# Kernel tuning notes

Measured on AMD Instinct MI355X. Metric: run time of the kernel, lower is better.

Reference implementation:

```python
import jax, jax.numpy as jnp
import numpy as np

DIM = 2048
N_HEADS = 16
N_KV_HEADS = 8
HEAD_DIM = DIM // N_HEADS  # 128
N_REP = N_HEADS // N_KV_HEADS
THETA = 10000.0


def _rope_cos_sin(seq_len, head_dim):
    # freqs_cis = polar(1, outer(t, 1/theta^(2i/d))), i in [0, head_dim//2)
    inv = 1.0 / (THETA ** (jnp.arange(0, head_dim, 2, dtype=jnp.float32) / head_dim))
    t = jnp.arange(seq_len, dtype=jnp.float32)
    freqs = jnp.outer(t, inv)  # [S, hd/2]
    return jnp.cos(freqs), jnp.sin(freqs)


def _apply_rope(x, cos, sin):
    # x: [B, S, H, hd]; pairs (even, odd) treated as complex and multiplied by e^{i*freq}
    xr = x[..., 0::2]
    xi = x[..., 1::2]
    c = cos[None, :, None, :]
    s = sin[None, :, None, :]
    out_r = xr * c - xi * s
    out_i = xr * s + xi * c
    return jnp.stack([out_r, out_i], axis=-1).reshape(x.shape)


def setup_inputs() -> dict:
    key = jax.random.key(0)
    ks = jax.random.split(key, 5)
    B, S = 2, 2048
    sc = 0.02
    return {
        "x": jax.random.normal(ks[0], (B, S, DIM), dtype=jnp.float32),
        "wq": jax.random.normal(ks[1], (N_HEADS * HEAD_DIM, DIM), dtype=jnp.float32) * sc,
        "wk": jax.random.normal(ks[2], (N_KV_HEADS * HEAD_DIM, DIM), dtype=jnp.float32) * sc,
        "wv": jax.random.normal(ks[3], (N_KV_HEADS * HEAD_DIM, DIM), dtype=jnp.float32) * sc,
        "wo": jax.random.normal(ks[4], (DIM, N_HEADS * HEAD_DIM), dtype=jnp.float32) * sc,
        "start_pos": 0,
        "inference": 0,
    }


def reference(x, wq, wk, wv, wo, start_pos, inference):
    B, S, _ = x.shape
    xq = (x @ wq.T).reshape(B, S, N_HEADS, HEAD_DIM)
    xk = (x @ wk.T).reshape(B, S, N_KV_HEADS, HEAD_DIM)
    xv = (x @ wv.T).reshape(B, S, N_KV_HEADS, HEAD_DIM)

    cos, sin = _rope_cos_sin(S, HEAD_DIM)
    xq = _apply_rope(xq, cos, sin)
    xk = _apply_rope(xk, cos, sin)

    # repeat_kv (GQA): [B,S,Hkv,hd] -> [B,S,Hkv*n_rep,hd]
    xk = jnp.repeat(xk, N_REP, axis=2)
    xv = jnp.repeat(xv, N_REP, axis=2)

    q = xq.transpose(0, 2, 1, 3)  # [B,H,S,hd]
    k = xk.transpose(0, 2, 1, 3)
    v = xv.transpose(0, 2, 1, 3)

    scores = jnp.einsum("bhqd,bhkd->bhqk", q, k) / np.sqrt(HEAD_DIM).astype(np.float32)
    mask = jnp.triu(jnp.full((S, S), -jnp.inf, dtype=scores.dtype), k=1)
    scores = scores + mask
    probs = jax.nn.softmax(scores.astype(jnp.float32), axis=-1).astype(q.dtype)

    out = jnp.einsum("bhqk,bhkd->bhqd", probs, v)
    out = out.transpose(0, 2, 1, 3).reshape(B, S, N_HEADS * HEAD_DIM)
    return out @ wo.T
```

## Files before the change

kernel.cpp:

```cpp
#include <hip/hip_runtime.h>
#include <hip/hip_bf16.h>
#include <stdint.h>
#include <type_traits>

typedef __attribute__((ext_vector_type(4))) float   f32x4;
typedef __attribute__((ext_vector_type(8))) __bf16  bf16x8;
typedef __attribute__((ext_vector_type(4))) unsigned int u32x4;

#define B_   2
#define S_   2048
#define DIM_ 2048
#define NH_  16
#define NKV_ 8
#define HD_  128

__device__ inline unsigned short f2bf(float f) {
    unsigned u = __float_as_uint(f);
    unsigned r = (u + 0x7fffu + ((u >> 16) & 1u)) >> 16;
    return (unsigned short)r;
}
__device__ inline float bf2f(unsigned short s) {
    return __uint_as_float(((unsigned)s) << 16);
}

__global__ void k_convert(const float* __restrict__ x,  const float* __restrict__ wq,
                          const float* __restrict__ wk, const float* __restrict__ wv,
                          const float* __restrict__ wo,
                          unsigned short* __restrict__ xb,  unsigned short* __restrict__ wqkb,
                          unsigned short* __restrict__ wvb, unsigned short* __restrict__ wob)
{
    int i = blockIdx.x * blockDim.x + threadIdx.x;
    const int NX = 2097152, NWQ = 1048576, NWK = 524288, NWV = 524288, NWO = 1048576;
    const float* src; unsigned short* dst; int j = i;
    if (j < NX) { src = x; dst = xb; }
    else {
        j -= NX;
        if (j < NWQ) { src = wq; dst = wqkb; }
        else {
            j -= NWQ;
            if (j < NWK) { src = wk; dst = wqkb + (size_t)2048 * 2048; }
            else {
                j -= NWK;
                if (j < NWV) { src = wv; dst = wvb; }
                else { j -= NWV; if (j >= NWO) return; src = wo; dst = wob; }
            }
        }
    }
    float4 v = reinterpret_cast<const float4*>(src)[j];
    ushort4 o;
    o.x = f2bf(v.x); o.y = f2bf(v.y); o.z = f2bf(v.z); o.w = f2bf(v.w);
    reinterpret_cast<ushort4*>(dst)[j] = o;
}

__global__ void k_rope_table(float* __restrict__ tab)
{
    int t = blockIdx.x * blockDim.x + threadIdx.x;
    if (t >= S_ * 64) return;
    int i = t & 63;
    int s = t >> 6;
    float inv = expf(-((float)i / 64.0f) * 9.210340371976184f);
    float ang = (float)s * inv;
    tab[2 * t]     = cosf(ang);
    tab[2 * t + 1] = sinf(ang);
}


#define BAR  __builtin_amdgcn_s_barrier()
#define WLG  asm volatile("s_waitcnt lgkmcnt(0)" ::: "memory")
#define WVM4 asm volatile("s_waitcnt vmcnt(4)" ::: "memory")
#define WVM0 asm volatile("s_waitcnt vmcnt(0)" ::: "memory")

#define G_LDS(SRC, DST) __builtin_amdgcn_global_load_lds( \
    (const __attribute__((address_space(1))) void*)(SRC), \
    (__attribute__((address_space(3))) void*)(DST), 16, 0, 0)

#define STAGE(MATB, DBUF, HALF, KT) do { \
    const unsigned short* _s0 = ((MATB) ? pb0 : pa0) + (size_t)(HALF) * 128 * 2048 + (KT) * 64; \
    const unsigned short* _s1 = ((MATB) ? pb1 : pa1) + (size_t)(HALF) * 128 * 2048 + (KT) * 64; \
    G_LDS(_s0, lds + (MATB) * 32768 + (DBUF) * 16384 + (HALF) * 8192 + lo0); \
    G_LDS(_s1, lds + (MATB) * 32768 + (DBUF) * 16384 + (HALF) * 8192 + lo1); \
} while (0)

#define LDA(DBUF, MH) { \
    _Pragma("unroll") \
    for (int mf = 0; mf < 4; ++mf) { \
        _Pragma("unroll") \
        for (int kk = 0; kk < 2; ++kk) { \
            const int R = wm * 128 + (MH) * 64 + mf * 16 + lr; \
            afr[MH][mf][kk] = *reinterpret_cast<const bf16x8*>( \
                &lds[(DBUF) * 16384 + R * 64 + (((kk * 4 + g) ^ (lr & 7)) * 8)]); \
        } } }

#define LDB(DBUF, NH) { \
    _Pragma("unroll") \
    for (int nf = 0; nf < 2; ++nf) { \
        _Pragma("unroll") \
        for (int kk = 0; kk < 2; ++kk) { \
            const int R = wn * 64 + (NH) * 32 + nf * 16 + lr; \
            bfr[NH][nf][kk] = *reinterpret_cast<const bf16x8*>( \
                &lds[32768 + (DBUF) * 16384 + R * 64 + (((kk * 4 + g) ^ (lr & 7)) * 8)]); \
        } } }

#define MMA(MH, NH) { \
    __builtin_amdgcn_s_setprio(1); \
    _Pragma("unroll") \
    for (int mf = 0; mf < 4; ++mf) { \
        _Pragma("unroll") \
        for (int nf = 0; nf < 2; ++nf) { \
            _Pragma("unroll") \
            for (int kk = 0; kk < 2; ++kk) \
                acc[(MH) * 4 + mf][(NH) * 2 + nf] = __builtin_amdgcn_mfma_f32_16x16x32_bf16( \
                    afr[MH][mf][kk], bfr[NH][nf][kk], acc[(MH) * 4 + mf][(NH) * 2 + nf], 0, 0, 0); \
        } } \
    __builtin_amdgcn_s_setprio(0); }

template <int MODE>
__global__ __launch_bounds__(512, 2) void k_gemm256(
    const unsigned short* __restrict__ A0g, const unsigned short* __restrict__ B0g,
    const unsigned short* __restrict__ A1g, const unsigned short* __restrict__ B1g,
    unsigned short* __restrict__ Cq, unsigned short* __restrict__ Cv,
    float* __restrict__ Cf, const float* __restrict__ tab)
{
    __shared__ __attribute__((aligned(16))) unsigned short lds[65536];

    const int tid  = threadIdx.x;
    const int lane = tid & 63;
    const int wid  = tid >> 6;
    const int g    = lane >> 4;
    const int lr   = lane & 15;
    const int wm   = wid >> 2;
    const int wn   = wid & 3;

    const unsigned short *Ag, *Bg;
    int brow, bcol;
    bool isQK = true;
    if constexpr (MODE == 0) {
        int swz = (blockIdx.x & 7) * 32 + (blockIdx.x >> 3);
        if (swz < 192) { Ag = A0g; Bg = B0g; brow = (swz / 12) << 8; bcol = (swz % 12) << 8; }
        else { int ix = swz - 192; isQK = false; Ag = A1g; Bg = B1g; brow = (ix >> 4) << 8; bcol = (ix & 15) << 8; }
    } else {
        int swz = (blockIdx.x & 7) * 16 + (blockIdx.x >> 3);
        Ag = A0g; Bg = B0g; brow = (swz >> 3) << 8; bcol = (swz & 7) << 8;
    }

    const int E0 = wid * 512 + lane * 8;
    const int E1 = E0 + 4096;
    const int r0 = E0 >> 6, r1 = E1 >> 6;
    const int c0 = ((((E0 >> 3) & 7) ^ (r0 & 7)) * 8);
    const int c1 = ((((E1 >> 3) & 7) ^ (r1 & 7)) * 8);
    const unsigned short* pa0 = Ag + (size_t)(brow + r0) * 2048 + c0;
    const unsigned short* pa1 = Ag + (size_t)(brow + r1) * 2048 + c1;
    const unsigned short* pb0 = Bg + (size_t)(bcol + r0) * 2048 + c0;
    const unsigned short* pb1 = Bg + (size_t)(bcol + r1) * 2048 + c1;
    const int lo0 = wid * 512;
    const int lo1 = lo0 + 4096;

    f32x4 acc[8][4] = {};
    bf16x8 afr[2][4][2];
    bf16x8 bfr[2][2][2];

    STAGE(0, 0, 0, 0); STAGE(0, 0, 1, 0); STAGE(1, 0, 0, 0); STAGE(1, 0, 1, 0);
    STAGE(0, 1, 0, 1); STAGE(1, 1, 0, 1);
    WVM0; BAR;

    #pragma unroll 1
    for (int i = 0; i < 16; ++i) {
        const int kt1 = 2 * i + 1;
        int kt2 = 2 * i + 2;  if (kt2 >= 32) kt2 -= 32;
        int kt3 = 2 * i + 3;  if (kt3 >= 32) kt3 -= 32;
        LDA(0, 0); LDB(0, 0);
        STAGE(0, 1, 1, kt1);
        BAR; WLG; MMA(0, 0); BAR;
        LDA(0, 1);
        STAGE(1, 1, 1, kt1);
        BAR; WLG; MMA(1, 0); BAR;
        LDB(0, 1);
        STAGE(1, 0, 0, kt2);
        BAR; WLG; MMA(0, 1); BAR;
        STAGE(0, 0, 0, kt2);
        WVM4;
        BAR; WLG; MMA(1, 1); BAR;
        LDA(1, 0); LDB(1, 0);
        STAGE(0, 0, 1, kt2);
        BAR; WLG; MMA(0, 0); BAR;
        LDA(1, 1);
        STAGE(1, 0, 1, kt2);
        BAR; WLG; MMA(1, 0); BAR;
        LDB(1, 1);
        STAGE(1, 1, 0, kt3);
        BAR; WLG; MMA(0, 1); BAR;
        STAGE(0, 1, 0, kt3);
        WVM4;
        BAR; WLG; MMA(1, 1); BAR;
    }

    if constexpr (MODE == 1) {
        #pragma unroll
        for (int m = 0; m < 8; ++m)
            #pragma unroll
            for (int n = 0; n < 4; ++n)
                #pragma unroll
                for (int r = 0; r < 4; ++r) {
                    int row = brow + wm * 128 + (m >> 2) * 64 + (m & 3) * 16 + g * 4 + r;
                    int col = bcol + wn * 64 + (n >> 1) * 32 + (n & 1) * 16 + lr;
                    Cf[(size_t)row * 2048 + col] = acc[m][n][r];
                }
    } else if (isQK) {
        #pragma unroll
        for (int m = 0; m < 8; ++m) {
            #pragma unroll
            for (int n = 0; n < 4; ++n) {
                int col = bcol + wn * 64 + (n >> 1) * 32 + (n & 1) * 16 + lr;
                int ci  = (col & 127) >> 1;
                int row0 = brow + wm * 128 + (m >> 2) * 64 + (m & 3) * 16 + g * 4;
                #pragma unroll
                for (int r = 0; r < 4; ++r) {
                    int row = row0 + r;
                    int s   = row & (S_ - 1);
                    float2 cs = *reinterpret_cast<const float2*>(&tab[(s * 64 + ci) * 2]);
                    float v = acc[m][n][r];
                    float o = __shfl_xor(v, 1);
                    float res = (lane & 1) ? fmaf(o, cs.y, v * cs.x)
                                           : fmaf(v, cs.x, -(o * cs.y));
                    Cq[(size_t)row * 3072 + col] = f2bf(res);
                }
            }
        }
    } else {
        #pragma unroll
        for (int m = 0; m < 8; ++m)
            #pragma unroll
            for (int n = 0; n < 4; ++n)
                #pragma unroll
                for (int r = 0; r < 4; ++r) {
                    int row = brow + wm * 128 + (m >> 2) * 64 + (m & 3) * 16 + g * 4 + r;
                    int col = bcol + wn * 64 + (n >> 1) * 32 + (n & 1) * 16 + lr;
                    Cv[(size_t)row * 4096 + col] = f2bf(acc[m][n][r]);
                }
    }
}

__global__ __launch_bounds__(256, 2) void k_attn(
    const unsigned short* __restrict__ QK,
    const unsigned short* __restrict__ Vt,
    unsigned short* __restrict__ O)
{
    __shared__ __attribute__((aligned(16))) unsigned short Ks[64 * 128];
    __shared__ __attribute__((aligned(16))) unsigned short Vs[128 * 64];

    const int tid  = threadIdx.x;
    const int lane = tid & 63;
    const int wid  = tid >> 6;
    const int g    = lane >> 4;
    const int lr   = lane & 15;

    const int bid    = blockIdx.x;
    const int qt_raw = bid & 15;
    const int h      = (bid >> 4) & 15;
    const int b      = bid >> 8;
    const int qt     = b ? (15 - qt_raw) : qt_raw;
    const int hk     = h >> 1;
    const int q0w    = qt * 128 + wid * 32;

    bf16x8 qf[2][4];
    #pragma unroll
    for (int qb = 0; qb < 2; ++qb)
        #pragma unroll
        for (int c = 0; c < 4; ++c)
            qf[qb][c] = *reinterpret_cast<const bf16x8*>(
                QK + (size_t)(b * S_ + q0w + qb * 16 + lr) * 3072 + h * HD_ + c * 32 + g * 8);

    f32x4 o_acc[2][8] = {};
    float m_run[2] = {-INFINITY, -INFINITY};
    float l_run[2] = {0.f, 0.f};

    const float C2 = 1.4426950408889634f * 0.08838834764831845f;
    const int nt = 2 * qt + 2;
    const int srcb = (g & 1) * 32 + lr;
    const bool hig = g >> 1;

    for (int t = 0; t < nt; ++t) {
        const int kv0 = t * 64;
        __syncthreads();
        #pragma unroll
        for (int i4 = 0; i4 < 4; ++i4) {
            const int base = (i4 * 4 + wid) * 512;
            const int E = base + lane * 8;
            {
                int row = E >> 7, ch = (E >> 3) & 15;
                int col = ((ch ^ (row & 15)) * 8);
                __builtin_amdgcn_global_load_lds(
                    (const __attribute__((address_space(1))) void*)(
                        QK + (size_t)(b * S_ + kv0 + row) * 3072 + 2048 + hk * HD_ + col),
                    (__attribute__((address_space(3))) void*)(Ks + base), 16, 0, 0);
            }
            {
                int d = E >> 6, ch = (E >> 3) & 7;
                int kv = ((ch ^ (d & 7)) * 8);
                __builtin_amdgcn_global_load_lds(
                    (const __attribute__((address_space(1))) void*)(
                        Vt + (size_t)(hk * HD_ + d) * (B_ * S_) + b * S_ + kv0 + kv),
                    (__attribute__((address_space(3))) void*)(Vs + base), 16, 0, 0);
            }
        }
        __syncthreads();

        const bool active = kv0 < q0w + 32;
        if (active) {
            f32x4 sv[2][4] = {};
            #pragma unroll
            for (int c = 0; c < 4; ++c)
                #pragma unroll
                for (int kvb = 0; kvb < 4; ++kvb) {
                    bf16x8 kf = *reinterpret_cast<const bf16x8*>(
                        &Ks[(kvb * 16 + lr) * 128 + (((c * 4 + g) ^ lr) * 8)]);
                    #pragma unroll
                    for (int qb = 0; qb < 2; ++qb)
                        sv[qb][kvb] = __builtin_amdgcn_mfma_f32_16x16x32_bf16(
                            kf, qf[qb][c], sv[qb][kvb], 0, 0, 0);
                }

            if (kv0 + 63 > q0w) {
                #pragma unroll
                for (int qb = 0; qb < 2; ++qb) {
                    int qg = q0w + qb * 16 + lr;
                    #pragma unroll
                    for (int kvb = 0; kvb < 4; ++kvb) {
                        int kvg0 = kv0 + kvb * 16 + g * 4;
                        #pragma unroll
                        for (int r = 0; r < 4; ++r)
                            if (kvg0 + r > qg) sv[qb][kvb][r] = -INFINITY;
                    }
                }
            }

            float mt[2];
            #pragma unroll
            for (int qb = 0; qb < 2; ++qb) {
                float a  = fmaxf(fmaxf(sv[qb][0][0], sv[qb][0][1]), fmaxf(sv[qb][0][2], sv[qb][0][3]));
                float c2 = fmaxf(fmaxf(sv[qb][1][0], sv[qb][1][1]), fmaxf(sv[qb][1][2], sv[qb][1][3]));
                float c3 = fmaxf(fmaxf(sv[qb][2][0], sv[qb][2][1]), fmaxf(sv[qb][2][2], sv[qb][2][3]));
                float c4 = fmaxf(fmaxf(sv[qb][3][0], sv[qb][3][1]), fmaxf(sv[qb][3][2], sv[qb][3][3]));
                float m0 = fmaxf(fmaxf(a, c2), fmaxf(c3, c4));
                m0 = fmaxf(m0, __shfl_xor(m0, 16));
                m0 = fmaxf(m0, __shfl_xor(m0, 32));
                mt[qb] = m0;
            }

            bool need = (mt[0] > m_run[0] + 90.5f) | (mt[1] > m_run[1] + 90.5f);
            if (__any(need)) {
                #pragma unroll
                for (int qb = 0; qb < 2; ++qb) {
                    float mn = fmaxf(m_run[qb], mt[qb]);
                    float al = exp2f((m_run[qb] - mn) * C2);
                    m_run[qb] = mn;
                    l_run[qb] *= al;
                    #pragma unroll
                    for (int db = 0; db < 8; ++db)
                        #pragma unroll
                        for (int r = 0; r < 4; ++r)
                            o_acc[qb][db][r] *= al;
                }
            }

            unsigned pk[2][4][2];
            #pragma unroll
            for (int qb = 0; qb < 2; ++qb) {
                float mb2 = m_run[qb] * C2;
                float rs = 0.f;
                #pragma unroll
                for (int kvb = 0; kvb < 4; ++kvb) {
                    float p0 = exp2f(fmaf(sv[qb][kvb][0], C2, -mb2));
                    float p1 = exp2f(fmaf(sv[qb][kvb][1], C2, -mb2));
                    float p2 = exp2f(fmaf(sv[qb][kvb][2], C2, -mb2));
                    float p3 = exp2f(fmaf(sv[qb][kvb][3], C2, -mb2));
                    rs += (p0 + p1) + (p2 + p3);
                    pk[qb][kvb][0] = (unsigned)f2bf(p0) | ((unsigned)f2bf(p1) << 16);
                    pk[qb][kvb][1] = (unsigned)f2bf(p2) | ((unsigned)f2bf(p3) << 16);
                }
                rs += __shfl_xor(rs, 16);
                rs += __shfl_xor(rs, 32);
                l_run[qb] += rs;
            }

            #pragma unroll
            for (int kk = 0; kk < 2; ++kk) {
                u32x4 w[2];
                #pragma unroll
                for (int qb = 0; qb < 2; ++qb) {
                    unsigned a0 = (unsigned)__shfl((int)pk[qb][2 * kk][0], srcb);
                    unsigned a1 = (unsigned)__shfl((int)pk[qb][2 * kk][1], srcb);
                    unsigned a2 = (unsigned)__shfl((int)pk[qb][2 * kk][0], srcb + 16);
                    unsigned a3 = (unsigned)__shfl((int)pk[qb][2 * kk][1], srcb + 16);
                    unsigned b0 = (unsigned)__shfl((int)pk[qb][2 * kk + 1][0], srcb);
                    unsigned b1 = (unsigned)__shfl((int)pk[qb][2 * kk + 1][1], srcb);
                    unsigned b2 = (unsigned)__shfl((int)pk[qb][2 * kk + 1][0], srcb + 16);
                    unsigned b3 = (unsigned)__shfl((int)pk[qb][2 * kk + 1][1], srcb + 16);
                    w[qb][0] = hig ? b0 : a0;
                    w[qb][1] = hig ? b1 : a1;
                    w[qb][2] = hig ? b2 : a2;
                    w[qb][3] = hig ? b3 : a3;
                }
                #pragma unroll
                for (int db = 0; db < 8; ++db) {
                    bf16x8 vf = *reinterpret_cast<const bf16x8*>(
                        &Vs[(db * 16 + lr) * 64 + (((kk * 4 + g) ^ (lr & 7)) * 8)]);
                    #pragma unroll
                    for (int qb = 0; qb < 2; ++qb) {
                        bf16x8 pb = *reinterpret_cast<const bf16x8*>(&w[qb]);
                        o_acc[qb][db] = __builtin_amdgcn_mfma_f32_16x16x32_bf16(
                            vf, pb, o_acc[qb][db], 0, 0, 0);
                    }
                }
            }
        }
    }

    #pragma unroll
    for (int qb = 0; qb < 2; ++qb) {
        float inv = 1.f / l_run[qb];
        size_t rowb = ((size_t)(b * S_ + q0w + qb * 16 + lr) * NH_ + h) * HD_;
        #pragma unroll
        for (int db = 0; db < 8; ++db) {
            ushort4 o4;
            o4.x = f2bf(o_acc[qb][db][0] * inv);
            o4.y = f2bf(o_acc[qb][db][1] * inv);
            o4.z = f2bf(o_acc[qb][db][2] * inv);
            o4.w = f2bf(o_acc[qb][db][3] * inv);
            *reinterpret_cast<ushort4*>(&O[rowb + db * 16 + g * 4]) = o4;
        }
    }
}

extern "C" void kernel_launch(void* const* d_in, const int* in_sizes, int n_in,
                              void* d_out, int out_size, void* d_ws, size_t ws_size,
                              hipStream_t stream)
{
    const float* x  = (const float*)d_in[0];
    const float* wq = (const float*)d_in[1];
    const float* wk = (const float*)d_in[2];
    const float* wv = (const float*)d_in[3];
    const float* wo = (const float*)d_in[4];
    float* out = (float*)d_out;

    char* ws = (char*)d_ws;
    size_t off = 0;
    auto alloc = [&](size_t bytes) -> void* {
        void* p = ws + off;
        off += (bytes + 255) & ~(size_t)255;
        return p;
    };
    unsigned short* xb   = (unsigned short*)alloc((size_t)B_ * S_ * DIM_ * 2);
    unsigned short* wqkb = (unsigned short*)alloc((size_t)3072 * 2048 * 2);
    unsigned short* wvb  = (unsigned short*)alloc((size_t)1024 * 2048 * 2);
    unsigned short* wob  = (unsigned short*)alloc((size_t)DIM_ * DIM_ * 2);
    unsigned short* QKb  = (unsigned short*)alloc((size_t)B_ * S_ * 3072 * 2);
    unsigned short* Vtb  = (unsigned short*)alloc((size_t)1024 * B_ * S_ * 2);
    unsigned short* Ob   = (unsigned short*)alloc((size_t)B_ * S_ * NH_ * HD_ * 2);
    float* tab = (float*)alloc((size_t)S_ * 64 * 2 * 4);

    k_convert<<<20480, 256, 0, stream>>>(x, wq, wk, wv, wo, xb, wqkb, wvb, wob);
    k_rope_table<<<(S_ * 64 + 255) / 256, 256, 0, stream>>>(tab);
    k_gemm256<0><<<256, 512, 0, stream>>>(xb, wqkb, wvb, xb, QKb, Vtb, nullptr, tab);
    k_attn<<<B_ * NH_ * (S_ / 128), 256, 0, stream>>>(QKb, Vtb, Ob);
    k_gemm256<1><<<128, 512, 0, stream>>>(Ob, wob, nullptr, nullptr, nullptr, nullptr, out, tab);

    (void)in_sizes; (void)n_in; (void)out_size; (void)ws_size;
}
```

Before: 234.1 us.

## Double-buffer K/V tiles in attention kernel and raise MFMA wave priority

The attention kernel now keeps two LDS buffers for K and V. It prefetches the next KV tile with global_load_lds while the current tile is computed, and waits with vmcnt(8) instead of issuing loads and then blocking on them. s_setprio is raised around the MFMA loops so matrix work gets scheduling preference. Doubling LDS to 64 KB per block may lower occupancy below the 2 blocks per CU the launch bounds request. The extra barriers per iteration add sync cost.

New measurement: 241.3 us. 3.1% more time.

```diff
diff --git a/kernel.cpp b/kernel.cpp
--- a/kernel.cpp
+++ b/kernel.cpp
@@ -64,11 +64,11 @@
     tab[2 * t + 1] = sinf(ang);
 }
 
-
 #define BAR  __builtin_amdgcn_s_barrier()
 #define WLG  asm volatile("s_waitcnt lgkmcnt(0)" ::: "memory")
 #define WVM4 asm volatile("s_waitcnt vmcnt(4)" ::: "memory")
 #define WVM0 asm volatile("s_waitcnt vmcnt(0)" ::: "memory")
+#define WVM8 asm volatile("s_waitcnt vmcnt(8)" ::: "memory")
 
 #define G_LDS(SRC, DST) __builtin_amdgcn_global_load_lds( \
     (const __attribute__((address_space(1))) void*)(SRC), \
@@ -245,8 +245,8 @@
     const unsigned short* __restrict__ Vt,
     unsigned short* __restrict__ O)
 {
-    __shared__ __attribute__((aligned(16))) unsigned short Ks[64 * 128];
-    __shared__ __attribute__((aligned(16))) unsigned short Vs[128 * 64];
+    __shared__ __attribute__((aligned(16))) unsigned short Ks[2][64 * 128];
+    __shared__ __attribute__((aligned(16))) unsigned short Vs[2][128 * 64];
 
     const int tid  = threadIdx.x;
     const int lane = tid & 63;
@@ -270,6 +270,7 @@
             qf[qb][c] = *reinterpret_cast<const bf16x8*>(
                 QK + (size_t)(b * S_ + q0w + qb * 16 + lr) * 3072 + h * HD_ + c * 32 + g * 8);
 
+    const int base_ = wid * 512;
     f32x4 o_acc[2][8] = {};
     float m_run[2] = {-INFINITY, -INFINITY};
     float l_run[2] = {0.f, 0.f};
@@ -279,46 +280,53 @@
     const int srcb = (g & 1) * 32 + lr;
     const bool hig = g >> 1;
 
+#define ATTN_STAGE(T, P) do { \
+    const int kv0s = (T) * 64; \
+    _Pragma("unroll") \
+    for (int i4 = 0; i4 < 4; ++i4) { \
+        const int base = (i4 * 4 + wid) * 512; \
+        const int E = base + lane * 8; \
+        { int row = E >> 7, ch = (E >> 3) & 15; \
+          int col = ((ch ^ (row & 15)) * 8); \
+          G_LDS(QK + (size_t)(b * S_ + kv0s + row) * 3072 + 2048 + hk * HD_ + col, \
+                &Ks[P][base]); } \
+        { int d = E >> 6, ch = (E >> 3) & 7; \
+          int kv = ((ch ^ (d & 7)) * 8); \
+          G_LDS(Vt + (size_t)(hk * HD_ + d) * (B_ * S_) + b * S_ + kv0s + kv, \
+                &Vs[P][base]); } \
+    } \
+} while (0)
+
+    ATTN_STAGE(0, 0);
+
+    #pragma unroll 1
     for (int t = 0; t < nt; ++t) {
+        const int p = t & 1;
         const int kv0 = t * 64;
-        __syncthreads();
-        #pragma unroll
-        for (int i4 = 0; i4 < 4; ++i4) {
-            const int base = (i4 * 4 + wid) * 512;
-            const int E = base + lane * 8;
-            {
-                int row = E >> 7, ch = (E >> 3) & 15;
-                int col = ((ch ^ (row & 15)) * 8);
-                __builtin_amdgcn_global_load_lds(
-                    (const __attribute__((address_space(1))) void*)(
-                        QK + (size_t)(b * S_ + kv0 + row) * 3072 + 2048 + hk * HD_ + col),
-                    (__attribute__((address_space(3))) void*)(Ks + base), 16, 0, 0);
-            }
-            {
-                int d = E >> 6, ch = (E >> 3) & 7;
-                int kv = ((ch ^ (d & 7)) * 8);
-                __builtin_amdgcn_global_load_lds(
-                    (const __attribute__((address_space(1))) void*)(
-                        Vt + (size_t)(hk * HD_ + d) * (B_ * S_) + b * S_ + kv0 + kv),
-                    (__attribute__((address_space(3))) void*)(Vs + base), 16, 0, 0);
-            }
+        if (t + 1 < nt) {
+            ATTN_STAGE(t + 1, p ^ 1);
+            WVM8;
+        } else {
+            WVM0;
         }
-        __syncthreads();
+        BAR;
 
         const bool active = kv0 < q0w + 32;
         if (active) {
             f32x4 sv[2][4] = {};
+            __builtin_amdgcn_s_setprio(1);
             #pragma unroll
             for (int c = 0; c < 4; ++c)
                 #pragma unroll
                 for (int kvb = 0; kvb < 4; ++kvb) {
                     bf16x8 kf = *reinterpret_cast<const bf16x8*>(
-                        &Ks[(kvb * 16 + lr) * 128 + (((c * 4 + g) ^ lr) * 8)]);
+                        &Ks[p][(kvb * 16 + lr) * 128 + (((c * 4 + g) ^ lr) * 8)]);
                     #pragma unroll
                     for (int qb = 0; qb < 2; ++qb)
                         sv[qb][kvb] = __builtin_amdgcn_mfma_f32_16x16x32_bf16(
                             kf, qf[qb][c], sv[qb][kvb], 0, 0, 0);
                 }
+            __builtin_amdgcn_s_setprio(0);
 
             if (kv0 + 63 > q0w) {
                 #pragma unroll
@@ -401,10 +409,11 @@
                     w[qb][2] = hig ? b2 : a2;
                     w[qb][3] = hig ? b3 : a3;
                 }
+                __builtin_amdgcn_s_setprio(1);
                 #pragma unroll
                 for (int db = 0; db < 8; ++db) {
                     bf16x8 vf = *reinterpret_cast<const bf16x8*>(
-                        &Vs[(db * 16 + lr) * 64 + (((kk * 4 + g) ^ (lr & 7)) * 8)]);
+                        &Vs[p][(db * 16 + lr) * 64 + (((kk * 4 + g) ^ (lr & 7)) * 8)]);
                     #pragma unroll
                     for (int qb = 0; qb < 2; ++qb) {
                         bf16x8 pb = *reinterpret_cast<const bf16x8*>(&w[qb]);
@@ -412,8 +421,10 @@
                             vf, pb, o_acc[qb][db], 0, 0, 0);
                     }
                 }
+                __builtin_amdgcn_s_setprio(0);
             }
         }
+        BAR;
     }
 
     #pragma unroll
@@ -430,6 +441,7 @@
             *reinterpret_cast<ushort4*>(&O[rowb + db * 16 + g * 4]) = o4;
         }
     }
+#undef ATTN_STAGE
 }
 
 extern "C" void kernel_launch(void* const* d_in, const int* in_sizes, int n_in,
```

## Use 128-wide KV tiles in attention with per-wave diagonal bounds

Applied to the files above, without the earlier changes.

The attention kernel now stages 128 keys and values per iteration instead of 64, which halves the number of barrier-synchronized load rounds. On the diagonal tile, each wave limits its QK and PV MFMA work to the blocks it needs (kvbmax/kkmax), so the old inactive-tile check is gone. It also adds s_setprio around the MFMA sections and packs bf16 with v_cvt_pk_bf16_f32. The costs are a larger LDS footprint (64KB total), which may reduce occupancy below 2 blocks per CU, and more registers for the score tile.

Result: slower. 260.5 us (+11.3%).

```diff
diff --git a/kernel.cpp b/kernel.cpp
--- a/kernel.cpp
+++ b/kernel.cpp
@@ -63,7 +63,6 @@
     tab[2 * t]     = cosf(ang);
     tab[2 * t + 1] = sinf(ang);
 }
-
 
 #define BAR  __builtin_amdgcn_s_barrier()
 #define WLG  asm volatile("s_waitcnt lgkmcnt(0)" ::: "memory")
@@ -245,8 +244,8 @@
     const unsigned short* __restrict__ Vt,
     unsigned short* __restrict__ O)
 {
-    __shared__ __attribute__((aligned(16))) unsigned short Ks[64 * 128];
-    __shared__ __attribute__((aligned(16))) unsigned short Vs[128 * 64];
+    __shared__ __attribute__((aligned(16))) unsigned short Ks[128 * 128];
+    __shared__ __attribute__((aligned(16))) unsigned short Vs[128 * 128];
 
     const int tid  = threadIdx.x;
     const int lane = tid & 63;
@@ -275,144 +274,146 @@
     float l_run[2] = {0.f, 0.f};
 
     const float C2 = 1.4426950408889634f * 0.08838834764831845f;
-    const int nt = 2 * qt + 2;
     const int srcb = (g & 1) * 32 + lr;
     const bool hig = g >> 1;
 
-    for (int t = 0; t < nt; ++t) {
-        const int kv0 = t * 64;
+    #pragma unroll 1
+    for (int t = 0; t <= qt; ++t) {
+        const int kv0 = t * 128;
         __syncthreads();
         #pragma unroll
-        for (int i4 = 0; i4 < 4; ++i4) {
+        for (int i4 = 0; i4 < 8; ++i4) {
             const int base = (i4 * 4 + wid) * 512;
             const int E = base + lane * 8;
-            {
-                int row = E >> 7, ch = (E >> 3) & 15;
-                int col = ((ch ^ (row & 15)) * 8);
-                __builtin_amdgcn_global_load_lds(
-                    (const __attribute__((address_space(1))) void*)(
-                        QK + (size_t)(b * S_ + kv0 + row) * 3072 + 2048 + hk * HD_ + col),
-                    (__attribute__((address_space(3))) void*)(Ks + base), 16, 0, 0);
-            }
-            {
-                int d = E >> 6, ch = (E >> 3) & 7;
-                int kv = ((ch ^ (d & 7)) * 8);
-                __builtin_amdgcn_global_load_lds(
-                    (const __attribute__((address_space(1))) void*)(
-                        Vt + (size_t)(hk * HD_ + d) * (B_ * S_) + b * S_ + kv0 + kv),
-                    (__attribute__((address_space(3))) void*)(Vs + base), 16, 0, 0);
-            }
+            const int row = E >> 7;
+            const int ch  = (E >> 3) & 15;
+            const int sc  = (ch ^ (row & 15)) * 8;
+            G_LDS(QK + (size_t)(b * S_ + kv0 + row) * 3072 + 2048 + hk * HD_ + sc,
+                  &Ks[base]);
+            G_LDS(Vt + (size_t)(hk * HD_ + row) * (B_ * S_) + b * S_ + kv0 + sc,
+                  &Vs[base]);
         }
         __syncthreads();
 
-        const bool active = kv0 < q0w + 32;
-        if (active) {
-            f32x4 sv[2][4] = {};
-            #pragma unroll
-            for (int c = 0; c < 4; ++c)
-                #pragma unroll
-                for (int kvb = 0; kvb < 4; ++kvb) {
-                    bf16x8 kf = *reinterpret_cast<const bf16x8*>(
-                        &Ks[(kvb * 16 + lr) * 128 + (((c * 4 + g) ^ lr) * 8)]);
+        const bool diag   = (t == qt);
+        const int  kvbmax = diag ? (2 * wid + 2) : 8;
+        const int  kkmax  = diag ? (wid + 1)     : 4;
+
+        f32x4 sv[2][8] = {};
+        __builtin_amdgcn_s_setprio(1);
+        #pragma unroll
+        for (int c = 0; c < 4; ++c)
+            #pragma unroll
+            for (int kvb = 0; kvb < 8; ++kvb) {
+                if (kvb >= kvbmax) continue;
+                bf16x8 kf = *reinterpret_cast<const bf16x8*>(
+                    &Ks[(kvb * 16 + lr) * 128 + (((c * 4 + g) ^ lr) * 8)]);
+                #pragma unroll
+                for (int qb = 0; qb < 2; ++qb)
+                    sv[qb][kvb] = __builtin_amdgcn_mfma_f32_16x16x32_bf16(
+                        kf, qf[qb][c], sv[qb][kvb], 0, 0, 0);
+            }
+        __builtin_amdgcn_s_setprio(0);
+
+        if (diag) {
+            #pragma unroll
+            for (int qb = 0; qb < 2; ++qb) {
+                int qg = wid * 32 + qb * 16 + lr;
+                #pragma unroll
+                for (int kvb = 0; kvb < 8; ++kvb) {
+                    if (kvb >= kvbmax) continue;
+                    int kvg0 = kvb * 16 + g * 4;
                     #pragma unroll
-                    for (int qb = 0; qb < 2; ++qb)
-                        sv[qb][kvb] = __builtin_amdgcn_mfma_f32_16x16x32_bf16(
-                            kf, qf[qb][c], sv[qb][kvb], 0, 0, 0);
+                    for (int r = 0; r < 4; ++r)
+                        if (kvg0 + r > qg) sv[qb][kvb][r] = -INFINITY;
                 }
-
-            if (kv0 + 63 > q0w) {
+            }
+        }
+
+        float mt[2];
+        #pragma unroll
+        for (int qb = 0; qb < 2; ++qb) {
+            float m0 = -INFINITY;
+            #pragma unroll
+            for (int kvb = 0; kvb < 8; ++kvb) {
+                if (kvb >= kvbmax) continue;
+                m0 = fmaxf(m0, fmaxf(fmaxf(sv[qb][kvb][0], sv[qb][kvb][1]),
+                                     fmaxf(sv[qb][kvb][2], sv[qb][kvb][3])));
+            }
+            m0 = fmaxf(m0, __shfl_xor(m0, 16));
+            m0 = fmaxf(m0, __shfl_xor(m0, 32));
+            mt[qb] = m0;
+        }
+
+        bool need = (mt[0] > m_run[0] + 90.5f) | (mt[1] > m_run[1] + 90.5f);
+        if (__any(need)) {
+            #pragma unroll
+            for (int qb = 0; qb < 2; ++qb) {
+                float mn = fmaxf(m_run[qb], mt[qb]);
+                float al = exp2f((m_run[qb] - mn) * C2);
+                m_run[qb] = mn;
+                l_run[qb] *= al;
+                #pragma unroll
+                for (int db = 0; db < 8; ++db)
+                    #pragma unroll
+                    for (int r = 0; r < 4; ++r)
+                        o_acc[qb][db][r] *= al;
+            }
+        }
+
+        unsigned pk[2][8][2];
+        #pragma unroll
+        for (int qb = 0; qb < 2; ++qb) {
+            float mb2 = m_run[qb] * C2;
+            float rs = 0.f;
+            #pragma unroll
+            for (int kvb = 0; kvb < 8; ++kvb) {
+                if (kvb >= kvbmax) continue;
+                float p0 = exp2f(fmaf(sv[qb][kvb][0], C2, -mb2));
+                float p1 = exp2f(fmaf(sv[qb][kvb][1], C2, -mb2));
+                float p2 = exp2f(fmaf(sv[qb][kvb][2], C2, -mb2));
+                float p3 = exp2f(fmaf(sv[qb][kvb][3], C2, -mb2));
+                rs += (p0 + p1) + (p2 + p3);
+                asm("v_cvt_pk_bf16_f32 %0, %1, %2" : "=v"(pk[qb][kvb][0]) : "v"(p0), "v"(p1));
+                asm("v_cvt_pk_bf16_f32 %0, %1, %2" : "=v"(pk[qb][kvb][1]) : "v"(p2), "v"(p3));
+            }
+            rs += __shfl_xor(rs, 16);
+            rs += __shfl_xor(rs, 32);
+            l_run[qb] += rs;
+        }
+
+        #pragma unroll
+        for (int kk = 0; kk < 4; ++kk) {
+            if (kk >= kkmax) continue;
+            u32x4 w[2];
+            #pragma unroll
+            for (int qb = 0; qb < 2; ++qb) {
+                unsigned a0 = (unsigned)__shfl((int)pk[qb][2 * kk][0], srcb);
+                unsigned a1 = (unsigned)__shfl((int)pk[qb][2 * kk][1], srcb);
+                unsigned a2 = (unsigned)__shfl((int)pk[qb][2 * kk][0], srcb + 16);
+                unsigned a3 = (unsigned)__shfl((int)pk[qb][2 * kk][1], srcb + 16);
+                unsigned b0 = (unsigned)__shfl((int)pk[qb][2 * kk + 1][0], srcb);
+                unsigned b1 = (unsigned)__shfl((int)pk[qb][2 * kk + 1][1], srcb);
+                unsigned b2 = (unsigned)__shfl((int)pk[qb][2 * kk + 1][0], srcb + 16);
+                unsigned b3 = (unsigned)__shfl((int)pk[qb][2 * kk + 1][1], srcb + 16);
+                w[qb][0] = hig ? b0 : a0;
+                w[qb][1] = hig ? b1 : a1;
+                w[qb][2] = hig ? b2 : a2;
+                w[qb][3] = hig ? b3 : a3;
+            }
+            __builtin_amdgcn_s_setprio(1);
+            #pragma unroll
+            for (int db = 0; db < 8; ++db) {
+                bf16x8 vf = *reinterpret_cast<const bf16x8*>(
+                    &Vs[(db * 16 + lr) * 128 + (((kk * 4 + g) ^ lr) * 8)]);
                 #pragma unroll
                 for (int qb = 0; qb < 2; ++qb) {
-                    int qg = q0w + qb * 16 + lr;
-                    #pragma unroll
-                    for (int kvb = 0; kvb < 4; ++kvb) {
-                        int kvg0 = kv0 + kvb * 16 + g * 4;
-                        #pragma unroll
-                        for (int r = 0; r < 4; ++r)
-                            if (kvg0 + r > qg) sv[qb][kvb][r] = -INFINITY;
-                    }
+                    bf16x8 pb = *reinterpret_cast<const bf16x8*>(&w[qb]);
+                    o_acc[qb][db] = __builtin_amdgcn_mfma_f32_16x16x32_bf16(
+                        vf, pb, o_acc[qb][db], 0, 0, 0);
                 }
             }
-
-            float mt[2];
-            #pragma unroll
-            for (int qb = 0; qb < 2; ++qb) {
-                float a  = fmaxf(fmaxf(sv[qb][0][0], sv[qb][0][1]), fmaxf(sv[qb][0][2], sv[qb][0][3]));
-                float c2 = fmaxf(fmaxf(sv[qb][1][0], sv[qb][1][1]), fmaxf(sv[qb][1][2], sv[qb][1][3]));
-                float c3 = fmaxf(fmaxf(sv[qb][2][0], sv[qb][2][1]), fmaxf(sv[qb][2][2], sv[qb][2][3]));
-                float c4 = fmaxf(fmaxf(sv[qb][3][0], sv[qb][3][1]), fmaxf(sv[qb][3][2], sv[qb][3][3]));
-                float m0 = fmaxf(fmaxf(a, c2), fmaxf(c3, c4));
-                m0 = fmaxf(m0, __shfl_xor(m0, 16));
-                m0 = fmaxf(m0, __shfl_xor(m0, 32));
-                mt[qb] = m0;
-            }
-
-            bool need = (mt[0] > m_run[0] + 90.5f) | (mt[1] > m_run[1] + 90.5f);
-            if (__any(need)) {
-                #pragma unroll
-                for (int qb = 0; qb < 2; ++qb) {
-                    float mn = fmaxf(m_run[qb], mt[qb]);
-                    float al = exp2f((m_run[qb] - mn) * C2);
-                    m_run[qb] = mn;
-                    l_run[qb] *= al;
-                    #pragma unroll
-                    for (int db = 0; db < 8; ++db)
-                        #pragma unroll
-                        for (int r = 0; r < 4; ++r)
-                            o_acc[qb][db][r] *= al;
-                }
-            }
-
-            unsigned pk[2][4][2];
-            #pragma unroll
-            for (int qb = 0; qb < 2; ++qb) {
-                float mb2 = m_run[qb] * C2;
-                float rs = 0.f;
-                #pragma unroll
-                for (int kvb = 0; kvb < 4; ++kvb) {
-                    float p0 = exp2f(fmaf(sv[qb][kvb][0], C2, -mb2));
-                    float p1 = exp2f(fmaf(sv[qb][kvb][1], C2, -mb2));
-                    float p2 = exp2f(fmaf(sv[qb][kvb][2], C2, -mb2));
-                    float p3 = exp2f(fmaf(sv[qb][kvb][3], C2, -mb2));
-                    rs += (p0 + p1) + (p2 + p3);
-                    pk[qb][kvb][0] = (unsigned)f2bf(p0) | ((unsigned)f2bf(p1) << 16);
-                    pk[qb][kvb][1] = (unsigned)f2bf(p2) | ((unsigned)f2bf(p3) << 16);
-                }
-                rs += __shfl_xor(rs, 16);
-                rs += __shfl_xor(rs, 32);
-                l_run[qb] += rs;
-            }
-
-            #pragma unroll
-            for (int kk = 0; kk < 2; ++kk) {
-                u32x4 w[2];
-                #pragma unroll
-                for (int qb = 0; qb < 2; ++qb) {
-                    unsigned a0 = (unsigned)__shfl((int)pk[qb][2 * kk][0], srcb);
-                    unsigned a1 = (unsigned)__shfl((int)pk[qb][2 * kk][1], srcb);
-                    unsigned a2 = (unsigned)__shfl((int)pk[qb][2 * kk][0], srcb + 16);
-                    unsigned a3 = (unsigned)__shfl((int)pk[qb][2 * kk][1], srcb + 16);
-                    unsigned b0 = (unsigned)__shfl((int)pk[qb][2 * kk + 1][0], srcb);
-                    unsigned b1 = (unsigned)__shfl((int)pk[qb][2 * kk + 1][1], srcb);
-                    unsigned b2 = (unsigned)__shfl((int)pk[qb][2 * kk + 1][0], srcb + 16);
-                    unsigned b3 = (unsigned)__shfl((int)pk[qb][2 * kk + 1][1], srcb + 16);
-                    w[qb][0] = hig ? b0 : a0;
-                    w[qb][1] = hig ? b1 : a1;
-                    w[qb][2] = hig ? b2 : a2;
-                    w[qb][3] = hig ? b3 : a3;
-                }
-                #pragma unroll
-                for (int db = 0; db < 8; ++db) {
-                    bf16x8 vf = *reinterpret_cast<const bf16x8*>(
-                        &Vs[(db * 16 + lr) * 64 + (((kk * 4 + g) ^ (lr & 7)) * 8)]);
-                    #pragma unroll
-                    for (int qb = 0; qb < 2; ++qb) {
-                        bf16x8 pb = *reinterpret_cast<const bf16x8*>(&w[qb]);
-                        o_acc[qb][db] = __builtin_amdgcn_mfma_f32_16x16x32_bf16(
-                            vf, pb, o_acc[qb][db], 0, 0, 0);
-                    }
-                }
-            }
+            __builtin_amdgcn_s_setprio(0);
         }
     }
 
```

## Split attention work across eight waves with 16 query rows each

Applied to the files above, without the earlier changes.

The attention kernel now launches 512 threads per block, and each of the eight waves handles 16 query rows instead of 32. The K/V tile loads are spread over more waves, and per-wave register state (o_acc, sv, qf) halves, which should raise occupancy. MFMA sections are wrapped in s_setprio to favour matrix issue. The trade-off is that each K/V fragment read from LDS now feeds only one MFMA instead of two, so LDS read traffic per FLOP doubles.

Measured after the change: 227.8 us. 1.03x faster.

```diff
diff --git a/kernel.cpp b/kernel.cpp
--- a/kernel.cpp
+++ b/kernel.cpp
@@ -63,7 +63,6 @@
     tab[2 * t]     = cosf(ang);
     tab[2 * t + 1] = sinf(ang);
 }
-
 
 #define BAR  __builtin_amdgcn_s_barrier()
 #define WLG  asm volatile("s_waitcnt lgkmcnt(0)" ::: "memory")
@@ -240,7 +239,7 @@
     }
 }
 
-__global__ __launch_bounds__(256, 2) void k_attn(
+__global__ __launch_bounds__(512, 4) void k_attn(
     const unsigned short* __restrict__ QK,
     const unsigned short* __restrict__ Vt,
     unsigned short* __restrict__ O)
@@ -260,173 +259,147 @@
     const int b      = bid >> 8;
     const int qt     = b ? (15 - qt_raw) : qt_raw;
     const int hk     = h >> 1;
-    const int q0w    = qt * 128 + wid * 32;
-
-    bf16x8 qf[2][4];
+    const int q0w    = qt * 128 + wid * 16;
+
+    bf16x8 qf[4];
     #pragma unroll
-    for (int qb = 0; qb < 2; ++qb)
-        #pragma unroll
-        for (int c = 0; c < 4; ++c)
-            qf[qb][c] = *reinterpret_cast<const bf16x8*>(
-                QK + (size_t)(b * S_ + q0w + qb * 16 + lr) * 3072 + h * HD_ + c * 32 + g * 8);
-
-    f32x4 o_acc[2][8] = {};
-    float m_run[2] = {-INFINITY, -INFINITY};
-    float l_run[2] = {0.f, 0.f};
+    for (int c = 0; c < 4; ++c)
+        qf[c] = *reinterpret_cast<const bf16x8*>(
+            QK + (size_t)(b * S_ + q0w + lr) * 3072 + h * HD_ + c * 32 + g * 8);
+
+    f32x4 o_acc[8] = {};
+    float m_run = -INFINITY;
+    float l_run = 0.f;
 
     const float C2 = 1.4426950408889634f * 0.08838834764831845f;
     const int nt = 2 * qt + 2;
     const int srcb = (g & 1) * 32 + lr;
     const bool hig = g >> 1;
 
+    #pragma unroll 1
     for (int t = 0; t < nt; ++t) {
         const int kv0 = t * 64;
         __syncthreads();
         #pragma unroll
-        for (int i4 = 0; i4 < 4; ++i4) {
-            const int base = (i4 * 4 + wid) * 512;
+        for (int i4 = 0; i4 < 2; ++i4) {
+            const int base = (i4 * 8 + wid) * 512;
             const int E = base + lane * 8;
             {
                 int row = E >> 7, ch = (E >> 3) & 15;
                 int col = ((ch ^ (row & 15)) * 8);
-                __builtin_amdgcn_global_load_lds(
-                    (const __attribute__((address_space(1))) void*)(
-                        QK + (size_t)(b * S_ + kv0 + row) * 3072 + 2048 + hk * HD_ + col),
-                    (__attribute__((address_space(3))) void*)(Ks + base), 16, 0, 0);
+                G_LDS(QK + (size_t)(b * S_ + kv0 + row) * 3072 + 2048 + hk * HD_ + col,
+                      &Ks[base]);
             }
             {
                 int d = E >> 6, ch = (E >> 3) & 7;
                 int kv = ((ch ^ (d & 7)) * 8);
-                __builtin_amdgcn_global_load_lds(
-                    (const __attribute__((address_space(1))) void*)(
-                        Vt + (size_t)(hk * HD_ + d) * (B_ * S_) + b * S_ + kv0 + kv),
-                    (__attribute__((address_space(3))) void*)(Vs + base), 16, 0, 0);
+                G_LDS(Vt + (size_t)(hk * HD_ + d) * (B_ * S_) + b * S_ + kv0 + kv,
+                      &Vs[base]);
             }
         }
         __syncthreads();
 
-        const bool active = kv0 < q0w + 32;
+        const bool active = kv0 < q0w + 16;
         if (active) {
-            f32x4 sv[2][4] = {};
+            f32x4 sv[4] = {};
+            __builtin_amdgcn_s_setprio(1);
             #pragma unroll
             for (int c = 0; c < 4; ++c)
                 #pragma unroll
                 for (int kvb = 0; kvb < 4; ++kvb) {
                     bf16x8 kf = *reinterpret_cast<const bf16x8*>(
                         &Ks[(kvb * 16 + lr) * 128 + (((c * 4 + g) ^ lr) * 8)]);
+                    sv[kvb] = __builtin_amdgcn_mfma_f32_16x16x32_bf16(
+                        kf, qf[c], sv[kvb], 0, 0, 0);
+                }
+            __builtin_amdgcn_s_setprio(0);
+
+            if (kv0 + 63 > q0w) {
+                int qg = q0w + lr;
+                #pragma unroll
+                for (int kvb = 0; kvb < 4; ++kvb) {
+                    int kvg0 = kv0 + kvb * 16 + g * 4;
                     #pragma unroll
-                    for (int qb = 0; qb < 2; ++qb)
-                        sv[qb][kvb] = __builtin_amdgcn_mfma_f32_16x16x32_bf16(
-                            kf, qf[qb][c], sv[qb][kvb], 0, 0, 0);
-                }
-
-            if (kv0 + 63 > q0w) {
-                #pragma unroll
-                for (int qb = 0; qb < 2; ++qb) {
-                    int qg = q0w + qb * 16 + lr;
+                    for (int r = 0; r < 4; ++r)
+                        if (kvg0 + r > qg) sv[kvb][r] = -INFINITY;
+                }
+            }
+
+            float m0 = fmaxf(fmaxf(fmaxf(sv[0][0], sv[0][1]), fmaxf(sv[0][2], sv[0][3])),
+                             fmaxf(fmaxf(sv[1][0], sv[1][1]), fmaxf(sv[1][2], sv[1][3])));
+            m0 = fmaxf(m0, fmaxf(fmaxf(sv[2][0], sv[2][1]), fmaxf(sv[2][2], sv[2][3])));
+            m0 = fmaxf(m0, fmaxf(fmaxf(sv[3][0], sv[3][1]), fmaxf(sv[3][2], sv[3][3])));
+            m0 = fmaxf(m0, __shfl_xor(m0, 16));
+            m0 = fmaxf(m0, __shfl_xor(m0, 32));
+
+            if (__any(m0 > m_run + 90.5f)) {
+                float mn = fmaxf(m_run, m0);
+                float al = exp2f((m_run - mn) * C2);
+                m_run = mn;
+                l_run *= al;
+                #pragma unroll
+                for (int db = 0; db < 8; ++db)
                     #pragma unroll
-                    for (int kvb = 0; kvb < 4; ++kvb) {
-                        int kvg0 = kv0 + kvb * 16 + g * 4;
-                        #pragma unroll
-                        for (int r = 0; r < 4; ++r)
-                            if (kvg0 + r > qg) sv[qb][kvb][r] = -INFINITY;
-                    }
-                }
-            }
-
-            float mt[2];
-            #pragma unroll
-            for (int qb = 0; qb < 2; ++qb) {
-                float a  = fmaxf(fmaxf(sv[qb][0][0], sv[qb][0][1]), fmaxf(sv[qb][0][2], sv[qb][0][3]));
-                float c2 = fmaxf(fmaxf(sv[qb][1][0], sv[qb][1][1]), fmaxf(sv[qb][1][2], sv[qb][1][3]));
-                float c3 = fmaxf(fmaxf(sv[qb][2][0], sv[qb][2][1]), fmaxf(sv[qb][2][2], sv[qb][2][3]));
-                float c4 = fmaxf(fmaxf(sv[qb][3][0], sv[qb][3][1]), fmaxf(sv[qb][3][2], sv[qb][3][3]));
-                float m0 = fmaxf(fmaxf(a, c2), fmaxf(c3, c4));
-                m0 = fmaxf(m0, __shfl_xor(m0, 16));
-                m0 = fmaxf(m0, __shfl_xor(m0, 32));
-                mt[qb] = m0;
-            }
-
-            bool need = (mt[0] > m_run[0] + 90.5f) | (mt[1] > m_run[1] + 90.5f);
-            if (__any(need)) {
-                #pragma unroll
-                for (int qb = 0; qb < 2; ++qb) {
-                    float mn = fmaxf(m_run[qb], mt[qb]);
-                    float al = exp2f((m_run[qb] - mn) * C2);
-                    m_run[qb] = mn;
-                    l_run[qb] *= al;
-                    #pragma unroll
-                    for (int db = 0; db < 8; ++db)
-                        #pragma unroll
-                        for (int r = 0; r < 4; ++r)
-                            o_acc[qb][db][r] *= al;
-                }
-            }
-
-            unsigned pk[2][4][2];
-            #pragma unroll
-            for (int qb = 0; qb < 2; ++qb) {
-                float mb2 = m_run[qb] * C2;
-                float rs = 0.f;
-                #pragma unroll
-                for (int kvb = 0; kvb < 4; ++kvb) {
-                    float p0 = exp2f(fmaf(sv[qb][kvb][0], C2, -mb2));
-                    float p1 = exp2f(fmaf(sv[qb][kvb][1], C2, -mb2));
-                    float p2 = exp2f(fmaf(sv[qb][kvb][2], C2, -mb2));
-                    float p3 = exp2f(fmaf(sv[qb][kvb][3], C2, -mb2));
-                    rs += (p0 + p1) + (p2 + p3);
-                    pk[qb][kvb][0] = (unsigned)f2bf(p0) | ((unsigned)f2bf(p1) << 16);
-                    pk[qb][kvb][1] = (unsigned)f2bf(p2) | ((unsigned)f2bf(p3) << 16);
-                }
-                rs += __shfl_xor(rs, 16);
-                rs += __shfl_xor(rs, 32);
-                l_run[qb] += rs;
-            }
+                    for (int r = 0; r < 4; ++r)
+                        o_acc[db][r] *= al;
+            }
+
+            unsigned pk[4][2];
+            float mb2 = m_run * C2;
+            float rs = 0.f;
+            #pragma unroll
+            for (int kvb = 0; kvb < 4; ++kvb) {
+                float p0 = exp2f(fmaf(sv[kvb][0], C2, -mb2));
+                float p1 = exp2f(fmaf(sv[kvb][1], C2, -mb2));
+                float p2 = exp2f(fmaf(sv[kvb][2], C2, -mb2));
+                float p3 = exp2f(fmaf(sv[kvb][3], C2, -mb2));
+                rs += (p0 + p1) + (p2 + p3);
+                pk[kvb][0] = (unsigned)f2bf(p0) | ((unsigned)f2bf(p1) << 16);
+                pk[kvb][1] = (unsigned)f2bf(p2) | ((unsigned)f2bf(p3) << 16);
+            }
+            rs += __shfl_xor(rs, 16);
+            rs += __shfl_xor(rs, 32);
+            l_run += rs;
 
             #pragma unroll
             for (int kk = 0; kk < 2; ++kk) {
-                u32x4 w[2];
-                #pragma unroll
-                for (int qb = 0; qb < 2; ++qb) {
-                    unsigned a0 = (unsigned)__shfl((int)pk[qb][2 * kk][0], srcb);
-                    unsigned a1 = (unsigned)__shfl((int)pk[qb][2 * kk][1], srcb);
-                    unsigned a2 = (unsigned)__shfl((int)pk[qb][2 * kk][0], srcb + 16);
-                    unsigned a3 = (unsigned)__shfl((int)pk[qb][2 * kk][1], srcb + 16);
-                    unsigned b0 = (unsigned)__shfl((int)pk[qb][2 * kk + 1][0], srcb);
-                    unsigned b1 = (unsigned)__shfl((int)pk[qb][2 * kk + 1][1], srcb);
-                    unsigned b2 = (unsigned)__shfl((int)pk[qb][2 * kk + 1][0], srcb + 16);
-                    unsigned b3 = (unsigned)__shfl((int)pk[qb][2 * kk + 1][1], srcb + 16);
-                    w[qb][0] = hig ? b0 : a0;
-                    w[qb][1] = hig ? b1 : a1;
-                    w[qb][2] = hig ? b2 : a2;
-                    w[qb][3] = hig ? b3 : a3;
-                }
+                u32x4 w;
+                unsigned a0 = (unsigned)__shfl((int)pk[2 * kk][0], srcb);
+                unsigned a1 = (unsigned)__shfl((int)pk[2 * kk][1], srcb);
+                unsigned a2 = (unsigned)__shfl((int)pk[2 * kk][0], srcb + 16);
+                unsigned a3 = (unsigned)__shfl((int)pk[2 * kk][1], srcb + 16);
+                unsigned b0 = (unsigned)__shfl((int)pk[2 * kk + 1][0], srcb);
+                unsigned b1 = (unsigned)__shfl((int)pk[2 * kk + 1][1], srcb);
+                unsigned b2 = (unsigned)__shfl((int)pk[2 * kk + 1][0], srcb + 16);
+                unsigned b3 = (unsigned)__shfl((int)pk[2 * kk + 1][1], srcb + 16);
+                w[0] = hig ? b0 : a0;
+                w[1] = hig ? b1 : a1;
+                w[2] = hig ? b2 : a2;
+                w[3] = hig ? b3 : a3;
+                bf16x8 pb = *reinterpret_cast<const bf16x8*>(&w);
+                __builtin_amdgcn_s_setprio(1);
                 #pragma unroll
                 for (int db = 0; db < 8; ++db) {
                     bf16x8 vf = *reinterpret_cast<const bf16x8*>(
                         &Vs[(db * 16 + lr) * 64 + (((kk * 4 + g) ^ (lr & 7)) * 8)]);
-                    #pragma unroll
-                    for (int qb = 0; qb < 2; ++qb) {
-                        bf16x8 pb = *reinterpret_cast<const bf16x8*>(&w[qb]);
-                        o_acc[qb][db] = __builtin_amdgcn_mfma_f32_16x16x32_bf16(
-                            vf, pb, o_acc[qb][db], 0, 0, 0);
-                    }
-                }
+                    o_acc[db] = __builtin_amdgcn_mfma_f32_16x16x32_bf16(
+                        vf, pb, o_acc[db], 0, 0, 0);
+                }
+                __builtin_amdgcn_s_setprio(0);
             }
         }
     }
 
-    #pragma unroll
-    for (int qb = 0; qb < 2; ++qb) {
-        float inv = 1.f / l_run[qb];
-        size_t rowb = ((size_t)(b * S_ + q0w + qb * 16 + lr) * NH_ + h) * HD_;
+    {
+        float inv = 1.f / l_run;
+        size_t rowb = ((size_t)(b * S_ + q0w + lr) * NH_ + h) * HD_;
         #pragma unroll
         for (int db = 0; db < 8; ++db) {
             ushort4 o4;
-            o4.x = f2bf(o_acc[qb][db][0] * inv);
-            o4.y = f2bf(o_acc[qb][db][1] * inv);
-            o4.z = f2bf(o_acc[qb][db][2] * inv);
-            o4.w = f2bf(o_acc[qb][db][3] * inv);
+            o4.x = f2bf(o_acc[db][0] * inv);
+            o4.y = f2bf(o_acc[db][1] * inv);
+            o4.z = f2bf(o_acc[db][2] * inv);
+            o4.w = f2bf(o_acc[db][3] * inv);
             *reinterpret_cast<ushort4*>(&O[rowb + db * 16 + g * 4]) = o4;
         }
     }
@@ -462,7 +435,7 @@
     k_convert<<<20480, 256, 0, stream>>>(x, wq, wk, wv, wo, xb, wqkb, wvb, wob);
     k_rope_table<<<(S_ * 64 + 255) / 256, 256, 0, stream>>>(tab);
     k_gemm256<0><<<256, 512, 0, stream>>>(xb, wqkb, wvb, xb, QKb, Vtb, nullptr, tab);
-    k_attn<<<B_ * NH_ * (S_ / 128), 256, 0, stream>>>(QKb, Vtb, Ob);
+    k_attn<<<B_ * NH_ * (S_ / 128), 512, 0, stream>>>(QKb, Vtb, Ob);
     k_gemm256<1><<<128, 512, 0, stream>>>(Ob, wob, nullptr, nullptr, nullptr, nullptr, out, tab);
 
     (void)in_sizes; (void)n_in; (void)out_size; (void)ws_size;
```
